# Performance work log

Hardware: AMD Instinct MI355X
Metric: run time of the kernel (lower is better)

The kernel has to match this reference:

```python
import jax, jax.numpy as jnp
import numpy as np

B, C, H, W = 2, 64, 256, 256
SIZE, STRIDE = 8, 4
NUMS = (H - SIZE) // STRIDE + 1          # 63 patches per axis
L = NUMS * NUMS                           # 3969 patches
K2 = SIZE * SIZE                          # 64 pixels per patch
EPS = 1e-05
TABLE = (2 * NUMS - 1) * (2 * NUMS - 1)   # relative-position bias table size


def _unfold_idx():
    # linear pixel index for each (kernel-offset k, patch l): [K2, L]
    i0 = np.arange(NUMS) * STRIDE
    j0 = np.arange(NUMS) * STRIDE
    kh = np.arange(SIZE)
    kw = np.arange(SIZE)
    r = kh[:, None, None, None] + i0[None, None, :, None]   # [S,1,N,1]
    c = kw[None, :, None, None] + j0[None, None, None, :]   # [1,S,1,N]
    return (r * W + c).reshape(K2, L)


def _rel_pos_index():
    ch = np.arange(NUMS)
    cw = np.arange(NUMS)
    coords = np.stack(np.meshgrid(ch, cw, indexing='ij'))   # [2,N,N]
    cf = coords.reshape(2, -1)                               # [2,L]
    rc = (cf[:, :, None] - cf[:, None, :]).transpose(1, 2, 0).astype(np.int64)
    rc[:, :, 0] += NUMS - 1
    rc[:, :, 1] += NUMS - 1
    rc[:, :, 0] *= 2 * NUMS - 1
    return rc.sum(-1)                                        # [L,L]


_IDX_NP = _unfold_idx()
_IDX = jnp.asarray(_IDX_NP)
_RPI = jnp.asarray(_rel_pos_index())
_count_np = np.zeros(H * W, np.float32)
np.add.at(_count_np, _IDX_NP.ravel(), 1.0)
_COUNT = jnp.asarray(_count_np.reshape(1, 1, H, W))


def setup_inputs() -> dict:
    key = jax.random.key(0)
    ks = jax.random.split(key, 9)
    x = jax.random.normal(ks[0], (B, C, H, W), dtype=jnp.float32)
    mask = jnp.round(jax.random.uniform(ks[1], (B, 1, H, W), dtype=jnp.float32))
    fg_gamma = 0.1 * jax.random.normal(ks[2], (C,), dtype=jnp.float32)
    fg_beta = 0.1 * jax.random.normal(ks[3], (C,), dtype=jnp.float32)
    bg_gamma = 0.1 * jax.random.normal(ks[4], (C,), dtype=jnp.float32)
    bg_beta = 0.1 * jax.random.normal(ks[5], (C,), dtype=jnp.float32)
    w_fore = 0.02 * jax.random.normal(ks[6], (C, C, K2), dtype=jnp.float32)
    w_back = 0.02 * jax.random.normal(ks[7], (C, C, K2), dtype=jnp.float32)
    rpb_table = 0.02 * jax.random.normal(ks[8], (TABLE,), dtype=jnp.float32)
    return {"x": x, "mask": mask, "fg_gamma": fg_gamma, "fg_beta": fg_beta,
            "bg_gamma": bg_gamma, "bg_beta": bg_beta,
            "w_fore": w_fore, "w_back": w_back, "rpb_table": rpb_table}


def _unfold(t):
    # [B,Ct,H,W] -> [B,Ct,L,K2]  (gather patch pixels)
    b, ct = t.shape[0], t.shape[1]
    return t.reshape(b, ct, H * W)[:, :, _IDX].transpose(0, 1, 3, 2)


def _patch_mean_std(region, m):
    # region [B,Ct,L,K2], m [B,1,L,K2] -> mu, 'std' (actually variance, per source)
    num = m.sum(-1)                                   # [B,1,L]
    mu = region.sum(-1) / (num + EPS)                 # [B,Ct,L]
    var = ((region - m * mu[..., None]) ** 2).sum(-1) / (num + EPS)
    return mu, var


def reference(x, mask, fg_gamma, fg_beta, bg_gamma, bg_beta, w_fore, w_back, rpb_table):
    # mask is already HxW -> nearest interpolate is identity
    invm = 1.0 - mask
    background = x * invm
    foreground = x * mask
    unorm_bg = (background * (1.0 + bg_gamma[None, :, None, None])
                + bg_beta[None, :, None, None]) * invm

    pb = _unfold(background)          # [B,C,L,K2]
    pf = _unfold(foreground)
    pm = _unfold(mask)                # [B,1,L,K2]

    mb, sb = _patch_mean_std(pb, 1.0 - pm)
    mf, sf = _patch_mean_std(pf, pm)

    in_b = (pb - mb[..., None]) / sb[..., None] * (1.0 - pm) + mb[..., None] * pm
    in_f = (pf - mf[..., None]) / sf[..., None] * pm + mf[..., None] * (1.0 - pm)

    tok_b = jnp.einsum('bclk,dck->bdl', in_b, w_back)   # [B,C,L]
    tok_f = jnp.einsum('bclk,dck->bdl', in_f, w_fore)

    bias = rpb_table[_RPI.reshape(-1)].reshape(L, L)
    S = jax.nn.softmax(jnp.einsum('bcl,bcm->blm', tok_f, tok_b) + bias[None], axis=-1)

    new_std = jnp.einsum('blm,bcm->bcl', S, sb)[..., None]   # [B,C,L,1]
    new_pf = in_f * new_std + new_std                        # (source uses new_std twice)

    # fold: scatter-add overlapping patches back, divide by coverage count
    flat = new_pf.transpose(0, 1, 3, 2).reshape(B, C, K2 * L)
    folded = jnp.zeros((B, C, H * W), x.dtype).at[:, :, _IDX.reshape(-1)].add(flat)
    new_fg = folded.reshape(B, C, H, W) / _COUNT

    new_fg = (new_fg * (1.0 + fg_gamma[None, :, None, None])
              + fg_beta[None, :, None, None]) * mask
    return new_fg + unorm_bg
```

## Files before the change

### kernel.cpp

```cpp
#include <hip/hip_runtime.h>
#include <stdint.h>

#define L_   3969
#define LP   3972
#define EPS_ 1e-5f
#define LOG2E 1.4426950408889634f
#define MH   6
#define IMR  11

#define OFF_MF   0
#define OFF_SF   508416
#define OFF_MB   1016832
#define OFF_SB   1525248
#define OFF_TOKF 2033664
#define OFF_TOKB 2542080
#define OFF_PACC 3050496
#define OFF_PM   6100992
#define OFF_PD   6148656
#define OFF_WT   6196320
#define PART_SLICE 1016832

typedef __attribute__((ext_vector_type(8))) short bf16x8;
typedef __attribute__((ext_vector_type(4))) float f32x4;

__device__ __forceinline__ uint16_t bf16_rne(float f) {
    uint32_t u = __float_as_uint(f);
    return (uint16_t)((u + 0x7FFFu + ((u >> 16) & 1u)) >> 16);
}
__device__ __forceinline__ void split_bf16(float v, uint16_t& h, uint16_t& l) {
    uint32_t u = __float_as_uint(v);
    uint32_t hu = u & 0xFFFF0000u;
    h = (uint16_t)(hu >> 16);
    l = bf16_rne(v - __uint_as_float(hu));
}
__device__ __forceinline__ uint4 pack8(const uint16_t* s) {
    uint4 r;
    r.x = (uint32_t)s[0] | ((uint32_t)s[1] << 16);
    r.y = (uint32_t)s[2] | ((uint32_t)s[3] << 16);
    r.z = (uint32_t)s[4] | ((uint32_t)s[5] << 16);
    r.w = (uint32_t)s[6] | ((uint32_t)s[7] << 16);
    return r;
}
__device__ __forceinline__ uint32_t pkhi2(float a, float b) {
    return (__float_as_uint(a) >> 16) | (__float_as_uint(b) & 0xFFFF0000u);
}
__device__ __forceinline__ uint32_t pklo2(float a, float b) {
    float ra = a - __uint_as_float(__float_as_uint(a) & 0xFFFF0000u);
    float rb = b - __uint_as_float(__float_as_uint(b) & 0xFFFF0000u);
    uint32_t r;
    asm("v_cvt_pk_bf16_f32 %0, %1, %2" : "=v"(r) : "v"(ra), "v"(rb));
    return r;
}

__global__ void k0_w2(const float* __restrict__ wf, const float* __restrict__ wb,
                      float* __restrict__ ws) {
    int c = blockIdx.x, t = blockIdx.y;
    const float* w = t ? wb : wf;
    uint16_t* w2 = (uint16_t*)(ws + OFF_WT);
    int tid = threadIdx.x;
    int lane = tid & 63, dq = tid >> 6;
    int d = dq * 16 + (lane & 15), quad = lane >> 4;
    for (int kci = 0; kci < 2; ++kci) {
        int k = kci * 32 + quad * 8;
        const float* src = w + (size_t)(d * 64 + c) * 64 + k;
        uint16_t hb[8], lb[8];
#pragma unroll
        for (int j = 0; j < 8; ++j) split_bf16(src[j], hb[j], lb[j]);
        size_t base = ((size_t)(((t * 64 + c) * 2 + kci) * 4 + dq) * 2) * 512 + lane * 8;
        *(uint4*)(w2 + base) = pack8(hb);
        *(uint4*)(w2 + base + 512) = pack8(lb);
    }
}

__global__ void k1_stats(const float* __restrict__ x, const float* __restrict__ mask,
                         float* __restrict__ ws) {
    int i = blockIdx.x, c = blockIdx.y, b = blockIdx.z;
    __shared__ float xs[8 * 256];
    __shared__ float ms[8 * 256];
    __shared__ float pS[5][256];
    int t = threadIdx.x;
    const float* xr = x + (((b * 64 + c) * 256) + i * 4) * 256;
    const float* mr = mask + (b * 256 + i * 4) * 256;
#pragma unroll
    for (int r = 0; r < 8; ++r) {
        xs[r * 256 + t] = xr[r * 256 + t];
        ms[r * 256 + t] = mr[r * 256 + t];
    }
    __syncthreads();
    int q = t >> 6, j = t & 63;
    float Sa = 0, Qa = 0, Sf = 0, Qf = 0, Nf = 0;
    if (j < 63) {
#pragma unroll
        for (int rr = 0; rr < 2; ++rr) {
            int base = (q * 2 + rr) * 256 + j * 4;
#pragma unroll
            for (int cc = 0; cc < 8; ++cc) {
                float v = xs[base + cc], m = ms[base + cc];
                Sa += v; Qa += v * v; Sf += v * m; Qf += v * v * m; Nf += m;
            }
        }
    }
    pS[0][t] = Sa; pS[1][t] = Qa; pS[2][t] = Sf; pS[3][t] = Qf; pS[4][t] = Nf;
    __syncthreads();
    if (q == 0 && j < 63) {
        Sa = pS[0][j] + pS[0][j + 64] + pS[0][j + 128] + pS[0][j + 192];
        Qa = pS[1][j] + pS[1][j + 64] + pS[1][j + 128] + pS[1][j + 192];
        Sf = pS[2][j] + pS[2][j + 64] + pS[2][j + 128] + pS[2][j + 192];
        Qf = pS[3][j] + pS[3][j + 64] + pS[3][j + 128] + pS[3][j + 192];
        Nf = pS[4][j] + pS[4][j + 64] + pS[4][j + 128] + pS[4][j + 192];
        float nb = 64.0f - Nf;
        float muf = Sf / (Nf + EPS_);
        float vaf = (Qf - 2.f * muf * Sf + Nf * muf * muf) / (Nf + EPS_);
        float Sb = Sa - Sf, Qb = Qa - Qf;
        float mub = Sb / (nb + EPS_);
        float vab = (Qb - 2.f * mub * Sb + nb * mub * mub) / (nb + EPS_);
        int idx = (b * 64 + c) * LP + i * 63 + j;
        ws[OFF_MF + idx] = muf; ws[OFF_SF + idx] = vaf;
        ws[OFF_MB + idx] = mub; ws[OFF_SB + idx] = vab;
    }
}

__global__ __launch_bounds__(256)
void k2_tok(const float* __restrict__ x, const float* __restrict__ mask,
            const float* __restrict__ wsc, float* __restrict__ ws) {
    int il = blockIdx.x, kc = blockIdx.y, b = blockIdx.z;
    int tid = threadIdx.x;
    int jl = tid & 63;
    int q = tid >> 6;
    __shared__ uint16_t IN[2][4 * 64 * 72];
    const uint16_t* w2 = (const uint16_t*)(wsc + OFF_WT);

    bool lv = jl < 63;
    int lg = il * 63 + jl;

    uint32_t mbits[2] = {0u, 0u};
    if (lv) {
#pragma unroll
        for (int oi = 0; oi < 2; ++oi) {
            int o = q + oi * 4;
            const float* mp = mask + (size_t)b * 65536 + (il * 4 + o) * 256 + jl * 4;
            float4 m0 = *(const float4*)mp;
            float4 m1 = *(const float4*)(mp + 4);
            uint32_t bits = 0;
            bits |= (m0.x != 0.f) ? 1u : 0u;  bits |= (m0.y != 0.f) ? 2u : 0u;
            bits |= (m0.z != 0.f) ? 4u : 0u;  bits |= (m0.w != 0.f) ? 8u : 0u;
            bits |= (m1.x != 0.f) ? 16u : 0u; bits |= (m1.y != 0.f) ? 32u : 0u;
            bits |= (m1.z != 0.f) ? 64u : 0u; bits |= (m1.w != 0.f) ? 128u : 0u;
            mbits[oi] = bits;
        }
    }

    f32x4 acc[2][2][2];
#pragma unroll
    for (int t = 0; t < 2; ++t)
#pragma unroll
        for (int i2 = 0; i2 < 2; ++i2)
#pragma unroll
            for (int j2 = 0; j2 < 2; ++j2) acc[t][i2][j2] = (f32x4)(0.f);

    int lane = tid & 63;
    int quad = lane >> 4;
    int c16 = lane & 15;
    int wd = q >> 1, wl = q & 1;
    int c0 = kc * 16;

    float4 xa[2][2];
    if (!lv) {
        xa[0][0] = xa[0][1] = xa[1][0] = xa[1][1] = make_float4(0.f, 0.f, 0.f, 0.f);
    }
    float muF = 0.f, vaF = 1.f, muB = 0.f, vaB = 1.f;

#define K2_LOADCH(cc)                                                                \
    do {                                                                             \
        if (lv) {                                                                    \
            int si = (b * 64 + (cc)) * LP + lg;                                      \
            muF = wsc[OFF_MF + si]; vaF = wsc[OFF_SF + si];                          \
            muB = wsc[OFF_MB + si]; vaB = wsc[OFF_SB + si];                          \
            const float* xp0 = x + (size_t)(b * 64 + (cc)) * 65536 + (il * 4 + q) * 256 + jl * 4; \
            xa[0][0] = *(const float4*)xp0;                                          \
            xa[0][1] = *(const float4*)(xp0 + 4);                                    \
            xa[1][0] = *(const float4*)(xp0 + 1024);                                 \
            xa[1][1] = *(const float4*)(xp0 + 1028);                                 \
        }                                                                            \
    } while (0)

#define K2_PACKSTORE(bufsel)                                                         \
    do {                                                                             \
        float invF = lv ? (1.0f / vaF) : 0.f;                                        \
        float invB = lv ? (1.0f / vaB) : 0.f;                                        \
        float cmF = lv ? muF : 0.f;                                                  \
        float cmB = lv ? muB : 0.f;                                                  \
        _Pragma("unroll")                                                            \
        for (int oi = 0; oi < 2; ++oi) {                                             \
            float xv[8];                                                             \
            xv[0] = xa[oi][0].x; xv[1] = xa[oi][0].y;                                \
            xv[2] = xa[oi][0].z; xv[3] = xa[oi][0].w;                                \
            xv[4] = xa[oi][1].x; xv[5] = xa[oi][1].y;                                \
            xv[6] = xa[oi][1].z; xv[7] = xa[oi][1].w;                                \
            float fv[8], bv[8];                                                      \
            _Pragma("unroll")                                                        \
            for (int j = 0; j < 8; ++j) {                                            \
                bool mf = (mbits[oi] >> j) & 1;                                      \
                float v = xv[j];                                                     \
                fv[j] = mf ? (v - cmF) * invF : cmF;                                 \
                bv[j] = mf ? cmB : (v - cmB) * invB;                                 \
            }                                                                        \
            uint4 FH, FL, BH, BL;                                                    \
            FH.x = pkhi2(fv[0], fv[1]); FH.y = pkhi2(fv[2], fv[3]);                  \
            FH.z = pkhi2(fv[4], fv[5]); FH.w = pkhi2(fv[6], fv[7]);                  \
            FL.x = pklo2(fv[0], fv[1]); FL.y = pklo2(fv[2], fv[3]);                  \
            FL.z = pklo2(fv[4], fv[5]); FL.w = pklo2(fv[6], fv[7]);                  \
            BH.x = pkhi2(bv[0], bv[1]); BH.y = pkhi2(bv[2], bv[3]);                  \
            BH.z = pkhi2(bv[4], bv[5]); BH.w = pkhi2(bv[6], bv[7]);                  \
            BL.x = pklo2(bv[0], bv[1]); BL.y = pklo2(bv[2], bv[3]);                  \
            BL.z = pklo2(bv[4], bv[5]); BL.w = pklo2(bv[6], bv[7]);                  \
            uint16_t* dst = &IN[bufsel][jl * 72 + (q + oi * 4) * 8];                 \
            *(uint4*)(dst)         = FH;                                             \
            *(uint4*)(dst + 4608)  = FL;                                             \
            *(uint4*)(dst + 9216)  = BH;                                             \
            *(uint4*)(dst + 13824) = BL;                                             \
        }                                                                            \
    } while (0)

#define K2_MFMA(bufi, cch)                                                           \
    do {                                                                             \
        _Pragma("unroll")                                                            \
        for (int t = 0; t < 2; ++t) {                                                \
            _Pragma("unroll")                                                        \
            for (int kci = 0; kci < 2; ++kci) {                                      \
                bf16x8 Ah[2], Al[2];                                                 \
                _Pragma("unroll")                                                    \
                for (int dqi = 0; dqi < 2; ++dqi) {                                  \
                    const uint16_t* ab = w2 +                                        \
                        ((size_t)(((t * 64 + (cch)) * 2 + kci) * 4 + (wd * 2 + dqi)) * 2) * 512 + lane * 8; \
                    Ah[dqi] = *(const bf16x8*)ab;                                    \
                    Al[dqi] = *(const bf16x8*)(ab + 512);                            \
                }                                                                    \
                _Pragma("unroll")                                                    \
                for (int lt = 0; lt < 2; ++lt) {                                     \
                    const uint16_t* bp = &IN[bufi][(t * 2) * 4608 +                  \
                        (wl * 32 + lt * 16 + c16) * 72 + kci * 32 + quad * 8];       \
                    bf16x8 Bh = *(const bf16x8*)bp;                                  \
                    bf16x8 Bl = *(const bf16x8*)(bp + 4608);                         \
                    _Pragma("unroll")                                                \
                    for (int dqi = 0; dqi < 2; ++dqi) {                              \
                        acc[t][dqi][lt] = __builtin_amdgcn_mfma_f32_16x16x32_bf16(Ah[dqi], Bh, acc[t][dqi][lt], 0, 0, 0); \
                        acc[t][dqi][lt] = __builtin_amdgcn_mfma_f32_16x16x32_bf16(Ah[dqi], Bl, acc[t][dqi][lt], 0, 0, 0); \
                        acc[t][dqi][lt] = __builtin_amdgcn_mfma_f32_16x16x32_bf16(Al[dqi], Bh, acc[t][dqi][lt], 0, 0, 0); \
                    }                                                                \
                }                                                                    \
            }                                                                        \
        }                                                                            \
    } while (0)

    K2_LOADCH(c0);
    K2_PACKSTORE(0);
    K2_LOADCH(c0 + 1);
    __syncthreads();

#pragma unroll 2
    for (int ci = 0; ci < 16; ++ci) {
        int cur = ci & 1;
        if (ci < 15) {
            K2_PACKSTORE(cur ^ 1);
            if (ci < 14) K2_LOADCH(c0 + ci + 2);
        }
        K2_MFMA(cur, c0 + ci);
        __syncthreads();
    }
#undef K2_LOADCH
#undef K2_PACKSTORE
#undef K2_MFMA

    float* ST = (float*)&IN[0][0];
#pragma unroll
    for (int t = 0; t < 2; ++t) {
        __syncthreads();
#pragma unroll
        for (int dqi = 0; dqi < 2; ++dqi)
#pragma unroll
            for (int lt = 0; lt < 2; ++lt)
#pragma unroll
                for (int r = 0; r < 4; ++r)
                    ST[(wl * 32 + lt * 16 + c16) * 68 + (wd * 2 + dqi) * 16 + quad * 4 + r] =
                        acc[t][dqi][lt][r];
        __syncthreads();
        float* dst = ws + OFF_TOKF + (size_t)kc * PART_SLICE + ((t * 2 + b) * (size_t)LP) * 64;
        int d4 = (tid & 15) * 4;
#pragma unroll
        for (int pass = 0; pass < 4; ++pass) {
            int l = pass * 16 + (tid >> 4);
            if (l < 63)
                *(float4*)&dst[(size_t)(il * 63 + l) * 64 + d4] = *(float4*)&ST[l * 68 + d4];
        }
    }
}

__global__ void k2r_reduce(float* __restrict__ ws) {
    size_t i = ((size_t)blockIdx.x * 256 + threadIdx.x) * 4;
    float4 a0 = *(float4*)&ws[OFF_TOKF + i];
    float4 a1 = *(float4*)&ws[OFF_TOKF + PART_SLICE + i];
    float4 a2 = *(float4*)&ws[OFF_TOKF + 2 * PART_SLICE + i];
    float4 a3 = *(float4*)&ws[OFF_TOKF + 3 * PART_SLICE + i];
    a0.x += a1.x + a2.x + a3.x; a0.y += a1.y + a2.y + a3.y;
    a0.z += a1.z + a2.z + a3.z; a0.w += a1.w + a2.w + a3.w;
    *(float4*)&ws[OFF_TOKF + i] = a0;
}

__global__ __launch_bounds__(256)
void k3_attn(const float* __restrict__ wsc, const float* __restrict__ rpb,
             float* __restrict__ ws) {
    int il = blockIdx.x, imc = blockIdx.y, b = blockIdx.z;
    int tid = threadIdx.x;
    int w = tid >> 6, lane = tid & 63;
    int c16 = lane & 15, quad = lane >> 4;

    __shared__ uint16_t TFh[64 * 72], TFl[64 * 72];
    __shared__ uint16_t TBh[64 * 72];
    __shared__ uint16_t TBl[64 * 72];
    __shared__ uint16_t SB[64 * 72];
    __shared__ float bias_r[128];

    const float* TOKF = wsc + OFF_TOKF + (size_t)b * LP * 64;
    const float* TOKB = wsc + OFF_TOKB + (size_t)b * LP * 64;
    const float* SBg  = wsc + OFF_SB + (size_t)b * 64 * LP;

    {
        int jl = tid >> 2, cc = (tid & 3) * 16;
        bool v = jl < 63;
        const float* src = TOKF + (size_t)(il * 63 + jl) * 64 + cc;
        uint16_t hh[16], lo[16];
#pragma unroll
        for (int u = 0; u < 16; u += 4) {
            float4 f = v ? *(const float4*)(src + u) : make_float4(0.f, 0.f, 0.f, 0.f);
            split_bf16(f.x, hh[u], lo[u]);     split_bf16(f.y, hh[u + 1], lo[u + 1]);
            split_bf16(f.z, hh[u + 2], lo[u + 2]); split_bf16(f.w, hh[u + 3], lo[u + 3]);
        }
        *(uint4*)&TFh[jl * 72 + cc] = pack8(hh); *(uint4*)&TFh[jl * 72 + cc + 8] = pack8(hh + 8);
        *(uint4*)&TFl[jl * 72 + cc] = pack8(lo); *(uint4*)&TFl[jl * 72 + cc + 8] = pack8(lo + 8);
    }

    float mrun[4] = {-1e30f, -1e30f, -1e30f, -1e30f};
    float drun[4] = {0.f, 0.f, 0.f, 0.f};
    f32x4 acc2[4];
#pragma unroll
    for (int ct = 0; ct < 4; ++ct) acc2[ct] = (f32x4)(0.f);

    int im0 = imc * IMR;
    int im1 = min(63, im0 + IMR);
    for (int im = im0; im < im1; ++im) {
        __syncthreads();
        {
            int jm = tid >> 2, cc = (tid & 3) * 16;
            bool v = jm < 63;
            const float* src = TOKB + (size_t)(im * 63 + jm) * 64 + cc;
            uint16_t hh[16], lo[16];
#pragma unroll
            for (int u = 0; u < 16; u += 4) {
                float4 f = v ? *(const float4*)(src + u) : make_float4(0.f, 0.f, 0.f, 0.f);
                split_bf16(f.x, hh[u], lo[u]);     split_bf16(f.y, hh[u + 1], lo[u + 1]);
                split_bf16(f.z, hh[u + 2], lo[u + 2]); split_bf16(f.w, hh[u + 3], lo[u + 3]);
            }
            *(uint4*)&TBh[jm * 72 + cc] = pack8(hh); *(uint4*)&TBh[jm * 72 + cc + 8] = pack8(hh + 8);
            *(uint4*)&TBl[jm * 72 + cc] = pack8(lo); *(uint4*)&TBl[jm * 72 + cc + 8] = pack8(lo + 8);
        }
        {
            int c = tid >> 2, mm = (tid & 3) * 16;
            const float* src = SBg + (size_t)c * LP + im * 63 + mm;
            uint16_t sv[16];
#pragma unroll
            for (int u = 0; u < 16; ++u)
                sv[u] = (mm + u < 63) ? bf16_rne(src[u]) : (uint16_t)0;
            *(uint4*)&SB[c * 72 + mm] = pack8(sv); *(uint4*)&SB[c * 72 + mm + 8] = pack8(sv + 8);
        }
        if (tid < 125) bias_r[tid] = rpb[(il - im + 62) * 125 + tid];
        else if (tid < 128) bias_r[tid] = 0.f;
        __syncthreads();

        f32x4 Z[4];
#pragma unroll
        for (int jt = 0; jt < 4; ++jt) Z[jt] = (f32x4)(0.f);
#pragma unroll
        for (int kk = 0; kk < 2; ++kk) {
            bf16x8 Ah = *(bf16x8*)&TFh[(w * 16 + c16) * 72 + kk * 32 + quad * 8];
            bf16x8 Al = *(bf16x8*)&TFl[(w * 16 + c16) * 72 + kk * 32 + quad * 8];
#pragma unroll
            for (int jt = 0; jt < 4; ++jt) {
                bf16x8 Bh = *(bf16x8*)&TBh[(jt * 16 + c16) * 72 + kk * 32 + quad * 8];
                bf16x8 Bl = *(bf16x8*)&TBl[(jt * 16 + c16) * 72 + kk * 32 + quad * 8];
                Z[jt] = __builtin_amdgcn_mfma_f32_16x16x32_bf16(Ah, Bh, Z[jt], 0, 0, 0);
                Z[jt] = __builtin_amdgcn_mfma_f32_16x16x32_bf16(Ah, Bl, Z[jt], 0, 0, 0);
                Z[jt] = __builtin_amdgcn_mfma_f32_16x16x32_bf16(Al, Bh, Z[jt], 0, 0, 0);
            }
        }
        float zv[4][4];
#pragma unroll
        for (int jt = 0; jt < 4; ++jt) {
            int jm = jt * 16 + c16;
#pragma unroll
            for (int r = 0; r < 4; ++r) {
                int i = w * 16 + quad * 4 + r;
                zv[jt][r] = (jm == 63) ? -1e30f : (Z[jt][r] + bias_r[i - jm + 62]);
            }
        }
        float alphav[4];
        uint16_t pb[4][4];
#pragma unroll
        for (int r = 0; r < 4; ++r) {
            float v = fmaxf(fmaxf(zv[0][r], zv[1][r]), fmaxf(zv[2][r], zv[3][r]));
            v = fmaxf(v, __shfl_xor(v, 1));
            v = fmaxf(v, __shfl_xor(v, 2));
            v = fmaxf(v, __shfl_xor(v, 4));
            v = fmaxf(v, __shfl_xor(v, 8));
            float mnew = fmaxf(mrun[r], v);
            alphav[r] = exp2f((mrun[r] - mnew) * LOG2E);
            float s = 0.f;
#pragma unroll
            for (int jt = 0; jt < 4; ++jt) {
                float p = exp2f((zv[jt][r] - mnew) * LOG2E);
                uint16_t h = bf16_rne(p);
                pb[jt][r] = h;
                s += __uint_as_float((uint32_t)h << 16);
            }
            s += __shfl_xor(s, 1); s += __shfl_xor(s, 2);
            s += __shfl_xor(s, 4); s += __shfl_xor(s, 8);
            drun[r] = drun[r] * alphav[r] + s;
            mrun[r] = mnew;
        }
#pragma unroll
        for (int ct = 0; ct < 4; ++ct)
#pragma unroll
            for (int r = 0; r < 4; ++r) acc2[ct][r] *= alphav[r];

        __syncthreads();
#pragma unroll
        for (int jt = 0; jt < 4; ++jt)
#pragma unroll
            for (int r = 0; r < 4; ++r)
                TBh[(w * 16 + quad * 4 + r) * 72 + jt * 16 + c16] = pb[jt][r];
        __syncthreads();

#pragma unroll
        for (int kk = 0; kk < 2; ++kk) {
            bf16x8 Pf = *(bf16x8*)&TBh[(w * 16 + c16) * 72 + kk * 32 + quad * 8];
#pragma unroll
            for (int ct = 0; ct < 4; ++ct) {
                bf16x8 Sf = *(bf16x8*)&SB[(ct * 16 + c16) * 72 + kk * 32 + quad * 8];
                acc2[ct] = __builtin_amdgcn_mfma_f32_16x16x32_bf16(Pf, Sf, acc2[ct], 0, 0, 0);
            }
        }
    }
    float* PA = ws + OFF_PACC + ((imc * 2 + b) * (size_t)LP) * 64;
#pragma unroll
    for (int r = 0; r < 4; ++r) {
        int i = w * 16 + quad * 4 + r;
        if (i < 63) {
            int rl = il * 63 + i;
#pragma unroll
            for (int ct = 0; ct < 4; ++ct)
                PA[(size_t)rl * 64 + ct * 16 + c16] = acc2[ct][r];
            if (c16 == 0) {
                ws[OFF_PM + (imc * 2 + b) * LP + rl] = mrun[r];
                ws[OFF_PD + (imc * 2 + b) * LP + rl] = drun[r];
            }
        }
    }
}

__global__ void k3b_merge(float* __restrict__ ws) {
    int b = blockIdx.y;
    int l = blockIdx.x * 4 + (threadIdx.x >> 6);
    int c = threadIdx.x & 63;
    if (l >= L_) return;
    float M = -1e30f;
#pragma unroll
    for (int p = 0; p < MH; ++p)
        M = fmaxf(M, ws[OFF_PM + (p * 2 + b) * LP + l]);
    float denom = 0.f, num = 0.f;
#pragma unroll
    for (int p = 0; p < MH; ++p) {
        float w = exp2f((ws[OFF_PM + (p * 2 + b) * LP + l] - M) * LOG2E);
        denom += ws[OFF_PD + (p * 2 + b) * LP + l] * w;
        num += ws[OFF_PACC + ((p * 2 + b) * (size_t)LP + l) * 64 + c] * w;
    }
    ws[OFF_PACC + (b * (size_t)LP + l) * 64 + c] = num / denom;
}

__global__ void k4_fold(const float* __restrict__ x, const float* __restrict__ mask,
                        const float* __restrict__ fg_g, const float* __restrict__ fg_b,
                        const float* __restrict__ bg_g, const float* __restrict__ bg_b,
                        const float* __restrict__ wsc, float* __restrict__ out) {
    int gid = blockIdx.x * 256 + threadIdx.x;
    int col = gid & 255, r = (gid >> 8) & 255, c = (gid >> 16) & 63, b = gid >> 22;
    float xv = x[gid];
    float m = mask[b * 65536 + r * 256 + col];
    int imin = (r >= 4) ? ((r - 4) >> 2) : 0;
    int imax = min(62, r >> 2);
    int jmin = (col >= 4) ? ((col - 4) >> 2) : 0;
    int jmax = min(62, col >> 2);
    const float* MF = wsc + OFF_MF + (b * 64 + c) * LP;
    const float* SF = wsc + OFF_SF + (b * 64 + c) * LP;
    const float* NS = wsc + OFF_PACC + b * (size_t)LP * 64;
    float folded = 0.f;
    int cnt = (imax - imin + 1) * (jmax - jmin + 1);
    for (int i = imin; i <= imax; ++i)
        for (int j = jmin; j <= jmax; ++j) {
            int l = i * 63 + j;
            float mf = MF[l], sf = SF[l];
            float inf_ = (m != 0.f) ? (xv - mf) / sf : mf;
            folded += NS[l * 64 + c] * (inf_ + 1.f);
        }
    float invm = 1.f - m;
    float ub = (xv * invm * (1.f + bg_g[c]) + bg_b[c]) * invm;
    float nf = (folded / (float)cnt * (1.f + fg_g[c]) + fg_b[c]) * m;
    out[gid] = nf + ub;
}

extern "C" void kernel_launch(void* const* d_in, const int* in_sizes, int n_in,
                              void* d_out, int out_size, void* d_ws, size_t ws_size,
                              hipStream_t stream) {
    const float* x    = (const float*)d_in[0];
    const float* mask = (const float*)d_in[1];
    const float* fg_g = (const float*)d_in[2];
    const float* fg_b = (const float*)d_in[3];
    const float* bg_g = (const float*)d_in[4];
    const float* bg_b = (const float*)d_in[5];
    const float* wf   = (const float*)d_in[6];
    const float* wb   = (const float*)d_in[7];
    const float* rpb  = (const float*)d_in[8];
    float* ws = (float*)d_ws;
    float* out = (float*)d_out;

    k0_w2<<<dim3(64, 2), 256, 0, stream>>>(wf, wb, ws);
    k1_stats<<<dim3(63, 64, 2), 256, 0, stream>>>(x, mask, ws);
    k2_tok<<<dim3(63, 4, 2), 256, 0, stream>>>(x, mask, ws, ws);
    k2r_reduce<<<dim3(993), 256, 0, stream>>>(ws);
    k3_attn<<<dim3(63, MH, 2), 256, 0, stream>>>(ws, rpb, ws);
    k3b_merge<<<dim3(993, 2), 256, 0, stream>>>(ws);
    k4_fold<<<dim3(32768), 256, 0, stream>>>(x, mask, fg_g, fg_b, bg_g, bg_b, ws, out);
}
```

Measured before the change: 283.7 us.

## Precompute per-patch affine fold coefficients in channel-major layout

Adds a kernel that, for each patch and channel, precomputes ns/sf, ns-mf*ns/sf and ns*(mf+1) and transposes them into channel-major arrays. The fold kernel then sums at most four coefficient triples and applies a single affine expression, with no per-patch division and no strided reads of the [L,64] new_std array. This costs one extra small launch and extra workspace traffic, and it overwrites the token buffers in workspace, relying on them being dead by this point.

```diff
diff --git a/kernel.cpp b/kernel.cpp
--- a/kernel.cpp
+++ b/kernel.cpp
@@ -19,6 +19,10 @@
 #define OFF_PD   6148656
 #define OFF_WT   6196320
 #define PART_SLICE 1016832
+
+#define OFF_A    2033664
+#define OFF_B    2542080
+#define OFF_C    4067328
 
 typedef __attribute__((ext_vector_type(8))) short bf16x8;
 typedef __attribute__((ext_vector_type(4))) float f32x4;
@@ -486,6 +490,28 @@
     ws[OFF_PACC + (b * (size_t)LP + l) * 64 + c] = num / denom;
 }
 
+__global__ void k3c_coef(float* __restrict__ ws) {
+    int b = blockIdx.y;
+    int bl = blockIdx.x;
+    int tid = threadIdx.x;
+    __shared__ float T[3][4][65];
+    int ls = tid >> 6, c = tid & 63;
+    int l = bl * 4 + ls;
+    float ns = ws[OFF_PACC + ((size_t)b * LP + l) * 64 + c];
+    float mf = ws[OFF_MF + (size_t)(b * 64 + c) * LP + l];
+    float sf = ws[OFF_SF + (size_t)(b * 64 + c) * LP + l];
+    float a = ns / sf;
+    T[0][ls][c] = a;
+    T[1][ls][c] = ns - mf * a;
+    T[2][ls][c] = ns * (mf + 1.f);
+    __syncthreads();
+    int c2 = tid >> 2, l2 = tid & 3;
+    size_t o = (size_t)(b * 64 + c2) * LP + bl * 4 + l2;
+    ws[OFF_A + o] = T[0][l2][c2];
+    ws[OFF_B + o] = T[1][l2][c2];
+    ws[OFF_C + o] = T[2][l2][c2];
+}
+
 __global__ void k4_fold(const float* __restrict__ x, const float* __restrict__ mask,
                         const float* __restrict__ fg_g, const float* __restrict__ fg_b,
                         const float* __restrict__ bg_g, const float* __restrict__ bg_b,
@@ -498,21 +524,24 @@
     int imax = min(62, r >> 2);
     int jmin = (col >= 4) ? ((col - 4) >> 2) : 0;
     int jmax = min(62, col >> 2);
-    const float* MF = wsc + OFF_MF + (b * 64 + c) * LP;
-    const float* SF = wsc + OFF_SF + (b * 64 + c) * LP;
-    const float* NS = wsc + OFF_PACC + b * (size_t)LP * 64;
-    float folded = 0.f;
-    int cnt = (imax - imin + 1) * (jmax - jmin + 1);
-    for (int i = imin; i <= imax; ++i)
-        for (int j = jmin; j <= jmax; ++j) {
-            int l = i * 63 + j;
-            float mf = MF[l], sf = SF[l];
-            float inf_ = (m != 0.f) ? (xv - mf) / sf : mf;
-            folded += NS[l * 64 + c] * (inf_ + 1.f);
-        }
+    bool fi = imax > imin, fj = jmax > jmin;
+    int l00 = imin * 63 + jmin;
+    const float* Aa = wsc + OFF_A + (size_t)(b * 64 + c) * LP;
+    const float* Ba = wsc + OFF_B + (size_t)(b * 64 + c) * LP;
+    const float* Ca = wsc + OFF_C + (size_t)(b * 64 + c) * LP;
+    float a00 = Aa[l00],      b00 = Ba[l00],      c00 = Ca[l00];
+    float a01 = Aa[l00 + 1],  b01 = Ba[l00 + 1],  c01 = Ca[l00 + 1];
+    float a10 = Aa[l00 + 63], b10 = Ba[l00 + 63], c10 = Ca[l00 + 63];
+    float a11 = Aa[l00 + 64], b11 = Ba[l00 + 64], c11 = Ca[l00 + 64];
+    bool fij = fi && fj;
+    float SA = a00 + (fj ? a01 : 0.f) + (fi ? a10 : 0.f) + (fij ? a11 : 0.f);
+    float SBv = b00 + (fj ? b01 : 0.f) + (fi ? b10 : 0.f) + (fij ? b11 : 0.f);
+    float SCv = c00 + (fj ? c01 : 0.f) + (fi ? c10 : 0.f) + (fij ? c11 : 0.f);
+    float folded = (m != 0.f) ? (xv * SA + SBv) : SCv;
+    float rc = (fi ? 0.5f : 1.f) * (fj ? 0.5f : 1.f);
     float invm = 1.f - m;
     float ub = (xv * invm * (1.f + bg_g[c]) + bg_b[c]) * invm;
-    float nf = (folded / (float)cnt * (1.f + fg_g[c]) + fg_b[c]) * m;
+    float nf = (folded * rc * (1.f + fg_g[c]) + fg_b[c]) * m;
     out[gid] = nf + ub;
 }
 
@@ -537,5 +566,6 @@
     k2r_reduce<<<dim3(993), 256, 0, stream>>>(ws);
     k3_attn<<<dim3(63, MH, 2), 256, 0, stream>>>(ws, rpb, ws);
     k3b_merge<<<dim3(993, 2), 256, 0, stream>>>(ws);
+    k3c_coef<<<dim3(993, 2), 256, 0, stream>>>(ws);
     k4_fold<<<dim3(32768), 256, 0, stream>>>(x, mask, fg_g, fg_b, bg_g, bg_b, ws, out);
 }
```

Result: faster. 262.7 us (-7.4%).
